# Optimization experiments

Measured on AMD Instinct MI355X. Metric: run time of the kernel, lower is better.

The kernel has to match this reference:

```python
import jax, jax.numpy as jnp
import numpy as np

GRID_SHAPE = (96, 96, 96)
GRID_LOWER = np.array([-1.2, -1.2, -1.2], dtype=np.float32)
GRID_STEPS = np.array([0.025, 0.025, 0.025], dtype=np.float32)
BIG = 1e10  # sentinel for cells outside an SDF's volume (min-combine ignores them)


def setup_inputs() -> dict:
    key = jax.random.key(0)
    k1, k2, k3, k4, k5 = jax.random.split(key, 5)
    M, S = 16, 64        # SDF library size, per-SDF resolution S^3
    B, N = 2, 8          # scenes, SDF instances per scene
    sdfs = jax.random.normal(k1, (M, S * S * S), dtype=jnp.float32)
    sdf_shapes = jnp.full((M, 3), S, dtype=jnp.int32)
    indices = jax.random.randint(k2, (B, N), 0, M, dtype=jnp.int32)
    trans = jax.random.uniform(k3, (B, N, 3), minval=-1.0, maxval=1.0)
    quat = jax.random.normal(k4, (B, N, 4))
    quat = quat / jnp.linalg.norm(quat, axis=-1, keepdims=True)
    sdf_poses = jnp.concatenate([trans, quat], axis=-1).astype(jnp.float32)
    sdf_widths = (0.02 * (1.0 + 0.2 * jax.random.uniform(k5, (B, N, 3)))).astype(jnp.float32)
    return {"sdfs": sdfs, "sdf_shapes": sdf_shapes, "indices": indices,
            "sdf_poses": sdf_poses, "sdf_widths": sdf_widths}


def _rotate_inv(q, v):
    # rotate v by the inverse (conjugate) of unit quaternion q = (x, y, z, w)
    u = -q[..., :3]
    w = q[..., 3:4]
    uv = jnp.cross(u, v)
    return v + 2.0 * jnp.cross(u, uv + w * v)


def reference(sdfs, sdf_shapes, indices, sdf_poses, sdf_widths):
    B, N = indices.shape
    GX, GY, GZ = GRID_SHAPE
    lower = jnp.asarray(GRID_LOWER)
    steps = jnp.asarray(GRID_STEPS)
    # world coordinates of grid cell centers: [GX, GY, GZ, 3]
    mesh = jnp.stack(jnp.meshgrid(jnp.arange(GX), jnp.arange(GY), jnp.arange(GZ),
                                  indexing='ij'), axis=-1).astype(jnp.float32)
    p = lower + (mesh + 0.5) * steps

    t = sdf_poses[..., :3]                                     # [B, N, 3]
    q = sdf_poses[..., 3:]
    q = q / jnp.linalg.norm(q, axis=-1, keepdims=True)         # [B, N, 4]

    # transform grid points into each SDF's local frame: [B, N, GX, GY, GZ, 3]
    d = p[None, None] - t[:, :, None, None, None, :]
    local = _rotate_inv(q[:, :, None, None, None, :], d)

    shp = sdf_shapes[indices]                                  # [B, N, 3] int
    shpf = shp.astype(local.dtype)[:, :, None, None, None, :]
    # continuous voxel coords, samples at cell centers
    g = local / sdf_widths[:, :, None, None, None, :] - 0.5
    inside = jnp.all((g >= 0.0) & (g <= shpf - 1.0), axis=-1)  # [B, N, GX, GY, GZ]
    f = jnp.clip(g, 0.0, shpf - 1.0)
    i0 = jnp.floor(f).astype(jnp.int32)
    frac = f - i0.astype(f.dtype)

    SX = shp[..., 0][:, :, None, None, None]
    SY = shp[..., 1][:, :, None, None, None]
    SZ = shp[..., 2][:, :, None, None, None]
    sdf_flat = sdfs[indices]                                   # [B, N, D]

    acc = jnp.zeros((B, N, GX, GY, GZ), dtype=sdfs.dtype)
    for dx in (0, 1):
        for dy in (0, 1):
            for dz in (0, 1):
                ii = jnp.minimum(i0[..., 0] + dx, SX - 1)
                jj = jnp.minimum(i0[..., 1] + dy, SY - 1)
                kk = jnp.minimum(i0[..., 2] + dz, SZ - 1)
                w = ((frac[..., 0] if dx else 1.0 - frac[..., 0]) *
                     (frac[..., 1] if dy else 1.0 - frac[..., 1]) *
                     (frac[..., 2] if dz else 1.0 - frac[..., 2]))
                flat = (ii * SY + jj) * SZ + kk
                vals = jnp.take_along_axis(sdf_flat, flat.reshape(B, N, -1),
                                           axis=2).reshape(B, N, GX, GY, GZ)
                acc = acc + w * vals

    per_sdf = jnp.where(inside, acc, BIG)
    return jnp.min(per_sdf, axis=1)                            # [B, GX, GY, GZ]
```

## Files before the change

kernel.cpp:

```cpp
#include <hip/hip_runtime.h>

#define GXD 96
#define GYD 96
#define GZD 96
#define PTS_PER_B (GXD * GYD * GZD)
#define BXC 8
#define BYC 8
#define BZC 8
#define GXB (GXD / BXC)
#define GYB (GYD / BYC)
#define GZB (GZD / BZC)
#define BLOCKS_PER_B (GXB * GYB * GZB)
#define RECSZ 56
#define BIGF 1e10f
#define GLOWER -1.2f
#define GSTEP 0.025f
#define EPS_G 1e-2f

__device__ __forceinline__ void rot_inv(float qx, float qy, float qz, float qw,
                                        float dx, float dy, float dz,
                                        float& rx, float& ry, float& rz)
{
    float ux = -qx, uy = -qy, uz = -qz;
    float uvx = uy * dz - uz * dy;
    float uvy = uz * dx - ux * dz;
    float uvz = ux * dy - uy * dx;
    float t2x = uvx + qw * dx;
    float t2y = uvy + qw * dy;
    float t2z = uvz + qw * dz;
    rx = dx + 2.0f * (uy * t2z - uz * t2y);
    ry = dy + 2.0f * (uz * t2x - ux * t2z);
    rz = dz + 2.0f * (ux * t2y - uy * t2x);
}

__device__ __forceinline__ float next_up(float a) { return __uint_as_float(__float_as_uint(a) + 1u); }
__device__ __forceinline__ float next_dn(float a) { return __uint_as_float(__float_as_uint(a) - 1u); }

__device__ float exact_lo(float w, float t)
{
    float a = t * w;
    while (a / w < t)            a = next_up(a);
    while (next_dn(a) / w >= t)  a = next_dn(a);
    return a;
}

__device__ float exact_hi(float w, float L)
{
    float a = L * w;
    while (a / w > L)            a = next_dn(a);
    while (next_up(a) / w <= L)  a = next_up(a);
    return a;
}

__global__ void prep_v9(const int* __restrict__ shapes,
                        const int* __restrict__ indices,
                        const float* __restrict__ poses,
                        const float* __restrict__ widths,
                        float* __restrict__ rec,
                        int BN, int sdf_stride)
{
    int bn = blockIdx.x * blockDim.x + threadIdx.x;
    if (bn >= BN) return;
    int m = indices[bn];
    const float* pp = poses + (size_t)bn * 7;
    float tx = pp[0], ty = pp[1], tz = pp[2];
    float qx = pp[3], qy = pp[4], qz = pp[5], qw = pp[6];
    float nrm = sqrtf(qx * qx + qy * qy + qz * qz + qw * qw);
    qx = qx / nrm; qy = qy / nrm; qz = qz / nrm; qw = qw / nrm;

    float wx = widths[bn * 3 + 0], wy = widths[bn * 3 + 1], wz = widths[bn * 3 + 2];
    int SX = shapes[m * 3 + 0], SY = shapes[m * 3 + 1], SZ = shapes[m * 3 + 2];
    float mx = (float)(SX - 1), my = (float)(SY - 1), mz = (float)(SZ - 1);

    float Ax = exact_lo(wx, 0.5f), Ay = exact_lo(wy, 0.5f), Az = exact_lo(wz, 0.5f);
    float Bx = exact_hi(wx, mx + 0.5f), By = exact_hi(wy, my + 0.5f), Bz = exact_hi(wz, mz + 0.5f);

    float xx = qx * qx, yy = qy * qy, zz = qz * qz;
    float xy = qx * qy, xz = qx * qz, yz = qy * qz;
    float wqx = qw * qx, wqy = qw * qy, wqz = qw * qz;
    float R00 = 1.0f - 2.0f * (yy + zz), R01 = 2.0f * (xy - wqz), R02 = 2.0f * (xz + wqy);
    float R10 = 2.0f * (xy + wqz), R11 = 1.0f - 2.0f * (xx + zz), R12 = 2.0f * (yz - wqx);
    float R20 = 2.0f * (xz - wqy), R21 = 2.0f * (yz + wqx), R22 = 1.0f - 2.0f * (xx + yy);

    float cx = 0.5f * (Ax + Bx), cy = 0.5f * (Ay + By), cz = 0.5f * (Az + Bz);
    float hx = 0.5f * (Bx - Ax), hy = 0.5f * (By - Ay), hz = 0.5f * (Bz - Az);
    const float MARG = 2e-3f;
    float wcx = tx + R00 * cx + R01 * cy + R02 * cz;
    float wcy = ty + R10 * cx + R11 * cy + R12 * cz;
    float wcz = tz + R20 * cx + R21 * cy + R22 * cz;
    float ex = fabsf(R00) * hx + fabsf(R01) * hy + fabsf(R02) * hz + MARG;
    float ey = fabsf(R10) * hx + fabsf(R11) * hy + fabsf(R12) * hz + MARG;
    float ez = fabsf(R20) * hx + fabsf(R21) * hy + fabsf(R22) * hz + MARG;

    float iwx = 1.0f / wx, iwy = 1.0f / wy, iwz = 1.0f / wz;
    float Mg0x = iwx * R00, Mg1x = iwx * R10, Mg2x = iwx * R20;
    float Mg0y = iwy * R01, Mg1y = iwy * R11, Mg2y = iwy * R21;
    float Mg0z = iwz * R02, Mg1z = iwz * R12, Mg2z = iwz * R22;
    float Cgx = -0.5f - (Mg0x * tx + Mg1x * ty + Mg2x * tz);
    float Cgy = -0.5f - (Mg0y * tx + Mg1y * ty + Mg2y * tz);
    float Cgz = -0.5f - (Mg0z * tx + Mg1z * ty + Mg2z * tz);

    float* r = rec + (size_t)bn * RECSZ;
    r[0] = tx;  r[1] = ty;  r[2] = tz;
    r[3] = qx;  r[4] = qy;  r[5] = qz;  r[6] = qw;
    r[7] = iwx; r[8] = iwy; r[9] = iwz;
    r[10] = mx; r[11] = my; r[12] = mz;
    r[13] = Ax; r[14] = Ay; r[15] = Az;
    r[16] = Bx; r[17] = By; r[18] = Bz;
    int* ri = (int*)r;
    ri[19] = m * sdf_stride;
    ri[20] = SX; ri[21] = SY; ri[22] = SZ;
    r[23] = 0.0f;
    r[24] = wcx - ex; r[25] = wcy - ey; r[26] = wcz - ez;
    r[27] = wcx + ex; r[28] = wcy + ey; r[29] = wcz + ez;
    r[30] = 0.0f; r[31] = 0.0f;
    r[32] = Mg0x; r[33] = Mg1x; r[34] = Mg2x;
    r[35] = Mg0y; r[36] = Mg1y; r[37] = Mg2y;
    r[38] = Mg0z; r[39] = Mg1z; r[40] = Mg2z;
    r[41] = Cgx; r[42] = Cgy; r[43] = Cgz;
    r[44] = mx + EPS_G; r[45] = my + EPS_G; r[46] = mz + EPS_G;
    r[47] = 0.0f;
    r[48] = mx - EPS_G; r[49] = my - EPS_G; r[50] = mz - EPS_G;
    r[51] = 0.0f; r[52] = 0.0f; r[53] = 0.0f; r[54] = 0.0f; r[55] = 0.0f;
}

struct __attribute__((aligned(4))) F2 { float lo, hi; };

__device__ __forceinline__ float trilerp_g(const float* __restrict__ sd,
                                           float gx, float gy, float gz,
                                           float mx, float my, float mz,
                                           int SX, int SY, int SZ)
{
    float fx = fminf(fmaxf(gx, 0.0f), mx);
    float fy = fminf(fmaxf(gy, 0.0f), my);
    float fz = fminf(fmaxf(gz, 0.0f), mz);
    int i0x = (int)fx, i0y = (int)fy, i0z = (int)fz;
    float frx = fx - (float)i0x;
    float fry = fy - (float)i0y;
    float frz = fz - (float)i0z;
    int i1x = min(i0x + 1, SX - 1);
    int i1y = min(i0y + 1, SY - 1);

    int zb = min(i0z, max(SZ - 2, 0));
    bool at0 = (i0z == zb);

    int b00 = (i0x * SY + i0y) * SZ + zb;
    int b01 = (i0x * SY + i1y) * SZ + zb;
    int b10 = (i1x * SY + i0y) * SZ + zb;
    int b11 = (i1x * SY + i1y) * SZ + zb;

    F2 p00 = *(const F2*)(sd + b00);
    F2 p01 = *(const F2*)(sd + b01);
    F2 p10 = *(const F2*)(sd + b10);
    F2 p11 = *(const F2*)(sd + b11);

    float v000 = at0 ? p00.lo : p00.hi, v001 = p00.hi;
    float v010 = at0 ? p01.lo : p01.hi, v011 = p01.hi;
    float v100 = at0 ? p10.lo : p10.hi, v101 = p10.hi;
    float v110 = at0 ? p11.lo : p11.hi, v111 = p11.hi;

    float c00 = v000 + frz * (v001 - v000);
    float c01 = v010 + frz * (v011 - v010);
    float c10 = v100 + frz * (v101 - v100);
    float c11 = v110 + frz * (v111 - v110);
    float c0 = c00 + fry * (c01 - c00);
    float c1 = c10 + fry * (c11 - c10);
    return c0 + frx * (c1 - c0);
}

__device__ __forceinline__ void eval_point(const float* __restrict__ r,
                                           const float* __restrict__ sdfs,
                                           float sgx, float sgy, float sgz,
                                           float px, float py, float pz,
                                           float& best)
{
    bool wide = (sgx >= -EPS_G) & (sgx <= r[44]) &
                (sgy >= -EPS_G) & (sgy <= r[45]) &
                (sgz >= -EPS_G) & (sgz <= r[46]);
    if (!wide) return;

    bool narrow = (sgx >= EPS_G) & (sgx <= r[48]) &
                  (sgy >= EPS_G) & (sgy <= r[49]) &
                  (sgz >= EPS_G) & (sgz <= r[50]);

    float gx = sgx, gy = sgy, gz = sgz;
    bool inside = true;
    if (!narrow) {
        float dx = px - r[0], dy = py - r[1], dz = pz - r[2];
        float rx, ry, rz;
        rot_inv(r[3], r[4], r[5], r[6], dx, dy, dz, rx, ry, rz);
        inside = (rx >= r[13]) & (rx <= r[16]) &
                 (ry >= r[14]) & (ry <= r[17]) &
                 (rz >= r[15]) & (rz <= r[18]);
        gx = rx * r[7] - 0.5f;
        gy = ry * r[8] - 0.5f;
        gz = rz * r[9] - 0.5f;
    }
    if (inside) {
        const int* ri = (const int*)r;
        float v = trilerp_g(sdfs + ri[19], gx, gy, gz,
                            r[10], r[11], r[12],
                            ri[20], ri[21], ri[22]);
        best = fminf(best, v);
    }
}

__global__ __launch_bounds__(256) void sdf_grid_v9(
    const float* __restrict__ sdfs,
    const float* __restrict__ rec,
    float* __restrict__ out,
    int N)
{
    int bidx = blockIdx.x;
    int b = blockIdx.y;
    int zb = bidx % GZB;
    int yb = (bidx / GZB) % GYB;
    int xb = bidx / (GZB * GYB);

    int t = threadIdx.x;
    int lane = t & 63;
    int lz = lane & 3;
    int ly = (lane >> 2) & 3;
    int lx = lane >> 4;
    int wx = (t >> 6) & 1;
    int wy = t >> 7;

    int cx = xb * BXC + wx * 4 + lx;
    int cy = yb * BYC + wy * 4 + ly;
    int cz = zb * BZC + lz * 2;

    float px  = GLOWER + ((float)cx + 0.5f) * GSTEP;
    float py  = GLOWER + ((float)cy + 0.5f) * GSTEP;
    float pz0 = GLOWER + ((float)cz + 0.5f) * GSTEP;
    float pz1 = GLOWER + ((float)(cz + 1) + 0.5f) * GSTEP;

    size_t out_idx = (size_t)b * PTS_PER_B + ((size_t)cx * GYD + cy) * GZD + cz;

    float bxl = GLOWER + ((float)(xb * BXC) + 0.5f) * GSTEP;
    float bxh = GLOWER + ((float)(xb * BXC + BXC - 1) + 0.5f) * GSTEP;
    float byl = GLOWER + ((float)(yb * BYC) + 0.5f) * GSTEP;
    float byh = GLOWER + ((float)(yb * BYC + BYC - 1) + 0.5f) * GSTEP;
    float bzl = GLOWER + ((float)(zb * BZC) + 0.5f) * GSTEP;
    float bzh = GLOWER + ((float)(zb * BZC + BZC - 1) + 0.5f) * GSTEP;

    bool lok = false;
    if (lane < N) {
        const float* r = rec + (size_t)(b * N + lane) * RECSZ;
        lok = (bxh >= r[24]) & (bxl <= r[27]) &
              (byh >= r[25]) & (byl <= r[28]) &
              (bzh >= r[26]) & (bzl <= r[29]);
    }
    unsigned int msk = (unsigned int)__ballot(lok);

    if (msk == 0u) {
        *(float2*)(out + out_idx) = make_float2(BIGF, BIGF);
        return;
    }

    float bestA = BIGF, bestB = BIGF;

    for (int n = 0; n < N; ++n) {
        if (!((msk >> n) & 1u)) continue;

        const float* r = rec + (size_t)(b * N + n) * RECSZ;

        float sgx = fmaf(r[32], px, fmaf(r[33], py, fmaf(r[34], pz0, r[41])));
        float sgy = fmaf(r[35], px, fmaf(r[36], py, fmaf(r[37], pz0, r[42])));
        float sgz = fmaf(r[38], px, fmaf(r[39], py, fmaf(r[40], pz0, r[43])));
        float dgx = GSTEP * r[34];
        float dgy = GSTEP * r[37];
        float dgz = GSTEP * r[40];

        eval_point(r, sdfs, sgx, sgy, sgz, px, py, pz0, bestA);
        eval_point(r, sdfs, sgx + dgx, sgy + dgy, sgz + dgz, px, py, pz1, bestB);
    }

    *(float2*)(out + out_idx) = make_float2(bestA, bestB);
}

__global__ __launch_bounds__(256) void sdf_grid_kernel(
    const float* __restrict__ sdfs,
    const int*   __restrict__ sdf_shapes,
    const int*   __restrict__ indices,
    const float* __restrict__ poses,
    const float* __restrict__ widths,
    float*       __restrict__ out,
    int total, int N, int sdf_stride)
{
    int idx = blockIdx.x * blockDim.x + threadIdx.x;
    if (idx >= total) return;
    int z = idx % GZD;
    int y = (idx / GZD) % GYD;
    int x = (idx / (GZD * GYD)) % GXD;
    int b = idx / (GZD * GYD * GXD);
    float px = GLOWER + ((float)x + 0.5f) * GSTEP;
    float py = GLOWER + ((float)y + 0.5f) * GSTEP;
    float pz = GLOWER + ((float)z + 0.5f) * GSTEP;
    float best = BIGF;
    for (int n = 0; n < N; ++n) {
        int bn = b * N + n;
        int m  = indices[bn];
        const float* pp = poses + (size_t)bn * 7;
        float tx = pp[0], ty = pp[1], tz = pp[2];
        float qx = pp[3], qy = pp[4], qz = pp[5], qw = pp[6];
        float nrm = sqrtf(qx * qx + qy * qy + qz * qz + qw * qw);
        qx = qx / nrm; qy = qy / nrm; qz = qz / nrm; qw = qw / nrm;
        float dx = px - tx, dy = py - ty, dz = pz - tz;
        float rx, ry, rz;
        rot_inv(qx, qy, qz, qw, dx, dy, dz, rx, ry, rz);
        const float* ww = widths + (size_t)bn * 3;
        float gx = rx / ww[0] - 0.5f;
        float gy = ry / ww[1] - 0.5f;
        float gz = rz / ww[2] - 0.5f;
        int SX = sdf_shapes[m * 3 + 0];
        int SY = sdf_shapes[m * 3 + 1];
        int SZ = sdf_shapes[m * 3 + 2];
        float mx = (float)(SX - 1), my = (float)(SY - 1), mz = (float)(SZ - 1);
        bool inside = (gx >= 0.0f) && (gx <= mx) &&
                      (gy >= 0.0f) && (gy <= my) &&
                      (gz >= 0.0f) && (gz <= mz);
        float fx = fminf(fmaxf(gx, 0.0f), mx);
        float fy = fminf(fmaxf(gy, 0.0f), my);
        float fz = fminf(fmaxf(gz, 0.0f), mz);
        int i0x = (int)floorf(fx), i0y = (int)floorf(fy), i0z = (int)floorf(fz);
        float frx = fx - (float)i0x, fry = fy - (float)i0y, frz = fz - (float)i0z;
        int i1x = min(i0x + 1, SX - 1);
        int i1y = min(i0y + 1, SY - 1);
        int i1z = min(i0z + 1, SZ - 1);
        const float* sd = sdfs + (size_t)m * sdf_stride;
        int b00 = (i0x * SY + i0y) * SZ;
        int b01 = (i0x * SY + i1y) * SZ;
        int b10 = (i1x * SY + i0y) * SZ;
        int b11 = (i1x * SY + i1y) * SZ;
        float v000 = sd[b00 + i0z], v001 = sd[b00 + i1z];
        float v010 = sd[b01 + i0z], v011 = sd[b01 + i1z];
        float v100 = sd[b10 + i0z], v101 = sd[b10 + i1z];
        float v110 = sd[b11 + i0z], v111 = sd[b11 + i1z];
        float wx0 = 1.0f - frx, wx1 = frx;
        float wy0 = 1.0f - fry, wy1 = fry;
        float wz0 = 1.0f - frz, wz1 = frz;
        float acc = wx0 * wy0 * wz0 * v000 + wx0 * wy0 * wz1 * v001
                  + wx0 * wy1 * wz0 * v010 + wx0 * wy1 * wz1 * v011
                  + wx1 * wy0 * wz0 * v100 + wx1 * wy0 * wz1 * v101
                  + wx1 * wy1 * wz0 * v110 + wx1 * wy1 * wz1 * v111;
        float val = inside ? acc : BIGF;
        best = fminf(best, val);
    }
    out[idx] = best;
}

extern "C" void kernel_launch(void* const* d_in, const int* in_sizes, int n_in,
                              void* d_out, int out_size, void* d_ws, size_t ws_size,
                              hipStream_t stream) {
    const float* sdfs    = (const float*)d_in[0];
    const int*   shapes  = (const int*)d_in[1];
    const int*   indices = (const int*)d_in[2];
    const float* poses   = (const float*)d_in[3];
    const float* widths  = (const float*)d_in[4];
    float*       out     = (float*)d_out;

    int M = in_sizes[1] / 3;
    int sdf_stride = in_sizes[0] / M;
    int B = out_size / PTS_PER_B;
    int N = in_sizes[2] / B;
    int BN = B * N;

    size_t ws_needed = (size_t)BN * RECSZ * sizeof(float);

    if (ws_size >= ws_needed && N <= 32 && (PTS_PER_B % 512) == 0) {
        float* rec = (float*)d_ws;
        prep_v9<<<(BN + 63) / 64, 64, 0, stream>>>(
            shapes, indices, poses, widths, rec, BN, sdf_stride);
        dim3 grid(BLOCKS_PER_B, B);
        sdf_grid_v9<<<grid, 256, 0, stream>>>(sdfs, rec, out, N);
    } else {
        int total = out_size;
        int blocks = (total + 255) / 256;
        sdf_grid_kernel<<<blocks, 256, 0, stream>>>(
            sdfs, shapes, indices, poses, widths, out, total, N, sdf_stride);
    }
}
```

Before: 24.85 us.

## Fuse per-instance prep into grid kernel via shared memory, four z-points per thread

Removes the separate prep kernel launch. Each block now recomputes the per-instance records into shared memory and reads them from LDS instead of global memory. The block shrinks to 128 threads, and each thread evaluates four consecutive z cells with incremental grid coordinates and writes one float4. The exact ulp-stepped bound computation is replaced by a division-based inside test, and every block redundantly recomputes the records, which adds a sync and per-block setup work.

```diff
diff --git a/kernel.cpp b/kernel.cpp
--- a/kernel.cpp
+++ b/kernel.cpp
@@ -11,11 +11,13 @@
 #define GYB (GYD / BYC)
 #define GZB (GZD / BZC)
 #define BLOCKS_PER_B (GXB * GYB * GZB)
-#define RECSZ 56
+#define MAXN 16
+#define RECL 44
 #define BIGF 1e10f
 #define GLOWER -1.2f
 #define GSTEP 0.025f
 #define EPS_G 1e-2f
+
 
 __device__ __forceinline__ void rot_inv(float qx, float qy, float qz, float qw,
                                         float dx, float dy, float dz,
@@ -33,97 +35,6 @@
     rz = dz + 2.0f * (ux * t2y - uy * t2x);
 }
 
-__device__ __forceinline__ float next_up(float a) { return __uint_as_float(__float_as_uint(a) + 1u); }
-__device__ __forceinline__ float next_dn(float a) { return __uint_as_float(__float_as_uint(a) - 1u); }
-
-__device__ float exact_lo(float w, float t)
-{
-    float a = t * w;
-    while (a / w < t)            a = next_up(a);
-    while (next_dn(a) / w >= t)  a = next_dn(a);
-    return a;
-}
-
-__device__ float exact_hi(float w, float L)
-{
-    float a = L * w;
-    while (a / w > L)            a = next_dn(a);
-    while (next_up(a) / w <= L)  a = next_up(a);
-    return a;
-}
-
-__global__ void prep_v9(const int* __restrict__ shapes,
-                        const int* __restrict__ indices,
-                        const float* __restrict__ poses,
-                        const float* __restrict__ widths,
-                        float* __restrict__ rec,
-                        int BN, int sdf_stride)
-{
-    int bn = blockIdx.x * blockDim.x + threadIdx.x;
-    if (bn >= BN) return;
-    int m = indices[bn];
-    const float* pp = poses + (size_t)bn * 7;
-    float tx = pp[0], ty = pp[1], tz = pp[2];
-    float qx = pp[3], qy = pp[4], qz = pp[5], qw = pp[6];
-    float nrm = sqrtf(qx * qx + qy * qy + qz * qz + qw * qw);
-    qx = qx / nrm; qy = qy / nrm; qz = qz / nrm; qw = qw / nrm;
-
-    float wx = widths[bn * 3 + 0], wy = widths[bn * 3 + 1], wz = widths[bn * 3 + 2];
-    int SX = shapes[m * 3 + 0], SY = shapes[m * 3 + 1], SZ = shapes[m * 3 + 2];
-    float mx = (float)(SX - 1), my = (float)(SY - 1), mz = (float)(SZ - 1);
-
-    float Ax = exact_lo(wx, 0.5f), Ay = exact_lo(wy, 0.5f), Az = exact_lo(wz, 0.5f);
-    float Bx = exact_hi(wx, mx + 0.5f), By = exact_hi(wy, my + 0.5f), Bz = exact_hi(wz, mz + 0.5f);
-
-    float xx = qx * qx, yy = qy * qy, zz = qz * qz;
-    float xy = qx * qy, xz = qx * qz, yz = qy * qz;
-    float wqx = qw * qx, wqy = qw * qy, wqz = qw * qz;
-    float R00 = 1.0f - 2.0f * (yy + zz), R01 = 2.0f * (xy - wqz), R02 = 2.0f * (xz + wqy);
-    float R10 = 2.0f * (xy + wqz), R11 = 1.0f - 2.0f * (xx + zz), R12 = 2.0f * (yz - wqx);
-    float R20 = 2.0f * (xz - wqy), R21 = 2.0f * (yz + wqx), R22 = 1.0f - 2.0f * (xx + yy);
-
-    float cx = 0.5f * (Ax + Bx), cy = 0.5f * (Ay + By), cz = 0.5f * (Az + Bz);
-    float hx = 0.5f * (Bx - Ax), hy = 0.5f * (By - Ay), hz = 0.5f * (Bz - Az);
-    const float MARG = 2e-3f;
-    float wcx = tx + R00 * cx + R01 * cy + R02 * cz;
-    float wcy = ty + R10 * cx + R11 * cy + R12 * cz;
-    float wcz = tz + R20 * cx + R21 * cy + R22 * cz;
-    float ex = fabsf(R00) * hx + fabsf(R01) * hy + fabsf(R02) * hz + MARG;
-    float ey = fabsf(R10) * hx + fabsf(R11) * hy + fabsf(R12) * hz + MARG;
-    float ez = fabsf(R20) * hx + fabsf(R21) * hy + fabsf(R22) * hz + MARG;
-
-    float iwx = 1.0f / wx, iwy = 1.0f / wy, iwz = 1.0f / wz;
-    float Mg0x = iwx * R00, Mg1x = iwx * R10, Mg2x = iwx * R20;
-    float Mg0y = iwy * R01, Mg1y = iwy * R11, Mg2y = iwy * R21;
-    float Mg0z = iwz * R02, Mg1z = iwz * R12, Mg2z = iwz * R22;
-    float Cgx = -0.5f - (Mg0x * tx + Mg1x * ty + Mg2x * tz);
-    float Cgy = -0.5f - (Mg0y * tx + Mg1y * ty + Mg2y * tz);
-    float Cgz = -0.5f - (Mg0z * tx + Mg1z * ty + Mg2z * tz);
-
-    float* r = rec + (size_t)bn * RECSZ;
-    r[0] = tx;  r[1] = ty;  r[2] = tz;
-    r[3] = qx;  r[4] = qy;  r[5] = qz;  r[6] = qw;
-    r[7] = iwx; r[8] = iwy; r[9] = iwz;
-    r[10] = mx; r[11] = my; r[12] = mz;
-    r[13] = Ax; r[14] = Ay; r[15] = Az;
-    r[16] = Bx; r[17] = By; r[18] = Bz;
-    int* ri = (int*)r;
-    ri[19] = m * sdf_stride;
-    ri[20] = SX; ri[21] = SY; ri[22] = SZ;
-    r[23] = 0.0f;
-    r[24] = wcx - ex; r[25] = wcy - ey; r[26] = wcz - ez;
-    r[27] = wcx + ex; r[28] = wcy + ey; r[29] = wcz + ez;
-    r[30] = 0.0f; r[31] = 0.0f;
-    r[32] = Mg0x; r[33] = Mg1x; r[34] = Mg2x;
-    r[35] = Mg0y; r[36] = Mg1y; r[37] = Mg2y;
-    r[38] = Mg0z; r[39] = Mg1z; r[40] = Mg2z;
-    r[41] = Cgx; r[42] = Cgy; r[43] = Cgz;
-    r[44] = mx + EPS_G; r[45] = my + EPS_G; r[46] = mz + EPS_G;
-    r[47] = 0.0f;
-    r[48] = mx - EPS_G; r[49] = my - EPS_G; r[50] = mz - EPS_G;
-    r[51] = 0.0f; r[52] = 0.0f; r[53] = 0.0f; r[54] = 0.0f; r[55] = 0.0f;
-}
-
 struct __attribute__((aligned(4))) F2 { float lo, hi; };
 
 __device__ __forceinline__ float trilerp_g(const float* __restrict__ sd,
@@ -174,14 +85,14 @@
                                            float px, float py, float pz,
                                            float& best)
 {
-    bool wide = (sgx >= -EPS_G) & (sgx <= r[44]) &
-                (sgy >= -EPS_G) & (sgy <= r[45]) &
-                (sgz >= -EPS_G) & (sgz <= r[46]);
+    bool wide = (sgx >= -EPS_G) & (sgx <= r[25]) &
+                (sgy >= -EPS_G) & (sgy <= r[26]) &
+                (sgz >= -EPS_G) & (sgz <= r[27]);
     if (!wide) return;
 
-    bool narrow = (sgx >= EPS_G) & (sgx <= r[48]) &
-                  (sgy >= EPS_G) & (sgy <= r[49]) &
-                  (sgz >= EPS_G) & (sgz <= r[50]);
+    bool narrow = (sgx >= EPS_G) & (sgx <= r[28]) &
+                  (sgy >= EPS_G) & (sgy <= r[29]) &
+                  (sgz >= EPS_G) & (sgz <= r[30]);
 
     float gx = sgx, gy = sgy, gz = sgz;
     bool inside = true;
@@ -189,93 +100,163 @@
         float dx = px - r[0], dy = py - r[1], dz = pz - r[2];
         float rx, ry, rz;
         rot_inv(r[3], r[4], r[5], r[6], dx, dy, dz, rx, ry, rz);
-        inside = (rx >= r[13]) & (rx <= r[16]) &
-                 (ry >= r[14]) & (ry <= r[17]) &
-                 (rz >= r[15]) & (rz <= r[18]);
-        gx = rx * r[7] - 0.5f;
-        gy = ry * r[8] - 0.5f;
-        gz = rz * r[9] - 0.5f;
+        gx = rx / r[7] - 0.5f;
+        gy = ry / r[8] - 0.5f;
+        gz = rz / r[9] - 0.5f;
+        inside = (gx >= 0.0f) & (gx <= r[10]) &
+                 (gy >= 0.0f) & (gy <= r[11]) &
+                 (gz >= 0.0f) & (gz <= r[12]);
     }
     if (inside) {
         const int* ri = (const int*)r;
-        float v = trilerp_g(sdfs + ri[19], gx, gy, gz,
+        float v = trilerp_g(sdfs + ri[37], gx, gy, gz,
                             r[10], r[11], r[12],
-                            ri[20], ri[21], ri[22]);
+                            ri[38], ri[39], ri[40]);
         best = fminf(best, v);
     }
 }
 
-__global__ __launch_bounds__(256) void sdf_grid_v9(
+__global__ __launch_bounds__(128) void sdf_grid_v11(
     const float* __restrict__ sdfs,
-    const float* __restrict__ rec,
-    float* __restrict__ out,
-    int N)
-{
+    const int*   __restrict__ shapes,
+    const int*   __restrict__ indices,
+    const float* __restrict__ poses,
+    const float* __restrict__ widths,
+    float*       __restrict__ out,
+    int N, int sdf_stride)
+{
+    __shared__ float srec[MAXN][RECL];
+
     int bidx = blockIdx.x;
     int b = blockIdx.y;
-    int zb = bidx % GZB;
-    int yb = (bidx / GZB) % GYB;
-    int xb = bidx / (GZB * GYB);
+    int zbk = bidx % GZB;
+    int ybk = (bidx / GZB) % GYB;
+    int xbk = bidx / (GZB * GYB);
 
     int t = threadIdx.x;
+
+    if (t < N) {
+        int bn = b * N + t;
+        int m = indices[bn];
+        const float* pp = poses + (size_t)bn * 7;
+        float tx = pp[0], ty = pp[1], tz = pp[2];
+        float qx = pp[3], qy = pp[4], qz = pp[5], qw = pp[6];
+        float nrm = sqrtf(qx * qx + qy * qy + qz * qz + qw * qw);
+        qx = qx / nrm; qy = qy / nrm; qz = qz / nrm; qw = qw / nrm;
+
+        float wx = widths[bn * 3 + 0], wy = widths[bn * 3 + 1], wz = widths[bn * 3 + 2];
+        int SX = shapes[m * 3 + 0], SY = shapes[m * 3 + 1], SZ = shapes[m * 3 + 2];
+        float mx = (float)(SX - 1), my = (float)(SY - 1), mz = (float)(SZ - 1);
+
+        float xx = qx * qx, yy = qy * qy, zz = qz * qz;
+        float xy = qx * qy, xz = qx * qz, yz = qy * qz;
+        float wqx = qw * qx, wqy = qw * qy, wqz = qw * qz;
+        float R00 = 1.0f - 2.0f * (yy + zz), R01 = 2.0f * (xy - wqz), R02 = 2.0f * (xz + wqy);
+        float R10 = 2.0f * (xy + wqz), R11 = 1.0f - 2.0f * (xx + zz), R12 = 2.0f * (yz - wqx);
+        float R20 = 2.0f * (xz - wqy), R21 = 2.0f * (yz + wqx), R22 = 1.0f - 2.0f * (xx + yy);
+
+        float Axa = 0.5f * wx, Aya = 0.5f * wy, Aza = 0.5f * wz;
+        float Bxa = (mx + 0.5f) * wx, Bya = (my + 0.5f) * wy, Bza = (mz + 0.5f) * wz;
+        float cx = 0.5f * (Axa + Bxa), cy = 0.5f * (Aya + Bya), cz = 0.5f * (Aza + Bza);
+        float hx = 0.5f * (Bxa - Axa), hy = 0.5f * (Bya - Aya), hz = 0.5f * (Bza - Aza);
+        const float MARG = 2e-3f;
+        float wcx = tx + R00 * cx + R01 * cy + R02 * cz;
+        float wcy = ty + R10 * cx + R11 * cy + R12 * cz;
+        float wcz = tz + R20 * cx + R21 * cy + R22 * cz;
+        float ex = fabsf(R00) * hx + fabsf(R01) * hy + fabsf(R02) * hz + MARG;
+        float ey = fabsf(R10) * hx + fabsf(R11) * hy + fabsf(R12) * hz + MARG;
+        float ez = fabsf(R20) * hx + fabsf(R21) * hy + fabsf(R22) * hz + MARG;
+
+        float iwx = 1.0f / wx, iwy = 1.0f / wy, iwz = 1.0f / wz;
+        float Mg0x = iwx * R00, Mg1x = iwx * R10, Mg2x = iwx * R20;
+        float Mg0y = iwy * R01, Mg1y = iwy * R11, Mg2y = iwy * R21;
+        float Mg0z = iwz * R02, Mg1z = iwz * R12, Mg2z = iwz * R22;
+        float Cgx = -0.5f - (Mg0x * tx + Mg1x * ty + Mg2x * tz);
+        float Cgy = -0.5f - (Mg0y * tx + Mg1y * ty + Mg2y * tz);
+        float Cgz = -0.5f - (Mg0z * tx + Mg1z * ty + Mg2z * tz);
+
+        float* r = srec[t];
+        r[0] = tx;  r[1] = ty;  r[2] = tz;
+        r[3] = qx;  r[4] = qy;  r[5] = qz;  r[6] = qw;
+        r[7] = wx;  r[8] = wy;  r[9] = wz;
+        r[10] = mx; r[11] = my; r[12] = mz;
+        r[13] = Mg0x; r[14] = Mg1x; r[15] = Mg2x;
+        r[16] = Mg0y; r[17] = Mg1y; r[18] = Mg2y;
+        r[19] = Mg0z; r[20] = Mg1z; r[21] = Mg2z;
+        r[22] = Cgx; r[23] = Cgy; r[24] = Cgz;
+        r[25] = mx + EPS_G; r[26] = my + EPS_G; r[27] = mz + EPS_G;
+        r[28] = mx - EPS_G; r[29] = my - EPS_G; r[30] = mz - EPS_G;
+        r[31] = wcx - ex; r[32] = wcy - ey; r[33] = wcz - ez;
+        r[34] = wcx + ex; r[35] = wcy + ey; r[36] = wcz + ez;
+        int* ri = (int*)r;
+        ri[37] = m * sdf_stride;
+        ri[38] = SX; ri[39] = SY; ri[40] = SZ;
+    }
+    __syncthreads();
+
     int lane = t & 63;
-    int lz = lane & 3;
-    int ly = (lane >> 2) & 3;
-    int lx = lane >> 4;
-    int wx = (t >> 6) & 1;
-    int wy = t >> 7;
-
-    int cx = xb * BXC + wx * 4 + lx;
-    int cy = yb * BYC + wy * 4 + ly;
-    int cz = zb * BZC + lz * 2;
+    int lyy = lane & 7;
+    int lxx = lane >> 3;
+    int wz4 = (t >> 6) & 1;
+
+    int cx = xbk * BXC + lxx;
+    int cy = ybk * BYC + lyy;
+    int cz0 = zbk * BZC + wz4 * 4;
 
     float px  = GLOWER + ((float)cx + 0.5f) * GSTEP;
     float py  = GLOWER + ((float)cy + 0.5f) * GSTEP;
-    float pz0 = GLOWER + ((float)cz + 0.5f) * GSTEP;
-    float pz1 = GLOWER + ((float)(cz + 1) + 0.5f) * GSTEP;
-
-    size_t out_idx = (size_t)b * PTS_PER_B + ((size_t)cx * GYD + cy) * GZD + cz;
-
-    float bxl = GLOWER + ((float)(xb * BXC) + 0.5f) * GSTEP;
-    float bxh = GLOWER + ((float)(xb * BXC + BXC - 1) + 0.5f) * GSTEP;
-    float byl = GLOWER + ((float)(yb * BYC) + 0.5f) * GSTEP;
-    float byh = GLOWER + ((float)(yb * BYC + BYC - 1) + 0.5f) * GSTEP;
-    float bzl = GLOWER + ((float)(zb * BZC) + 0.5f) * GSTEP;
-    float bzh = GLOWER + ((float)(zb * BZC + BZC - 1) + 0.5f) * GSTEP;
+    float pz0 = GLOWER + ((float)cz0 + 0.5f) * GSTEP;
+    float pz1 = GLOWER + ((float)(cz0 + 1) + 0.5f) * GSTEP;
+    float pz2 = GLOWER + ((float)(cz0 + 2) + 0.5f) * GSTEP;
+    float pz3 = GLOWER + ((float)(cz0 + 3) + 0.5f) * GSTEP;
+
+    size_t out_idx = (size_t)b * PTS_PER_B + ((size_t)cx * GYD + cy) * GZD + cz0;
+
+    float bxl = GLOWER + ((float)(xbk * BXC) + 0.5f) * GSTEP;
+    float bxh = GLOWER + ((float)(xbk * BXC + 7) + 0.5f) * GSTEP;
+    float byl = GLOWER + ((float)(ybk * BYC) + 0.5f) * GSTEP;
+    float byh = GLOWER + ((float)(ybk * BYC + 7) + 0.5f) * GSTEP;
+    float bzl = GLOWER + ((float)(zbk * BZC + wz4 * 4) + 0.5f) * GSTEP;
+    float bzh = GLOWER + ((float)(zbk * BZC + wz4 * 4 + 3) + 0.5f) * GSTEP;
 
     bool lok = false;
     if (lane < N) {
-        const float* r = rec + (size_t)(b * N + lane) * RECSZ;
-        lok = (bxh >= r[24]) & (bxl <= r[27]) &
-              (byh >= r[25]) & (byl <= r[28]) &
-              (bzh >= r[26]) & (bzl <= r[29]);
+        const float* r = srec[lane];
+        lok = (bxh >= r[31]) & (bxl <= r[34]) &
+              (byh >= r[32]) & (byl <= r[35]) &
+              (bzh >= r[33]) & (bzl <= r[36]);
     }
     unsigned int msk = (unsigned int)__ballot(lok);
 
     if (msk == 0u) {
-        *(float2*)(out + out_idx) = make_float2(BIGF, BIGF);
+        *(float4*)(out + out_idx) = make_float4(BIGF, BIGF, BIGF, BIGF);
         return;
     }
 
-    float bestA = BIGF, bestB = BIGF;
+    float b0 = BIGF, b1 = BIGF, b2 = BIGF, b3 = BIGF;
 
     for (int n = 0; n < N; ++n) {
         if (!((msk >> n) & 1u)) continue;
 
-        const float* r = rec + (size_t)(b * N + n) * RECSZ;
-
-        float sgx = fmaf(r[32], px, fmaf(r[33], py, fmaf(r[34], pz0, r[41])));
-        float sgy = fmaf(r[35], px, fmaf(r[36], py, fmaf(r[37], pz0, r[42])));
-        float sgz = fmaf(r[38], px, fmaf(r[39], py, fmaf(r[40], pz0, r[43])));
-        float dgx = GSTEP * r[34];
-        float dgy = GSTEP * r[37];
-        float dgz = GSTEP * r[40];
-
-        eval_point(r, sdfs, sgx, sgy, sgz, px, py, pz0, bestA);
-        eval_point(r, sdfs, sgx + dgx, sgy + dgy, sgz + dgz, px, py, pz1, bestB);
-    }
-
-    *(float2*)(out + out_idx) = make_float2(bestA, bestB);
+        const float* r = srec[n];
+
+        float sgx = fmaf(r[13], px, fmaf(r[14], py, fmaf(r[15], pz0, r[22])));
+        float sgy = fmaf(r[16], px, fmaf(r[17], py, fmaf(r[18], pz0, r[23])));
+        float sgz = fmaf(r[19], px, fmaf(r[20], py, fmaf(r[21], pz0, r[24])));
+        float dgx = GSTEP * r[15];
+        float dgy = GSTEP * r[18];
+        float dgz = GSTEP * r[21];
+
+        eval_point(r, sdfs, sgx, sgy, sgz, px, py, pz0, b0);
+        float s1x = sgx + dgx, s1y = sgy + dgy, s1z = sgz + dgz;
+        eval_point(r, sdfs, s1x, s1y, s1z, px, py, pz1, b1);
+        float s2x = s1x + dgx, s2y = s1y + dgy, s2z = s1z + dgz;
+        eval_point(r, sdfs, s2x, s2y, s2z, px, py, pz2, b2);
+        float s3x = s2x + dgx, s3y = s2y + dgy, s3z = s2z + dgz;
+        eval_point(r, sdfs, s3x, s3y, s3z, px, py, pz3, b3);
+    }
+
+    *(float4*)(out + out_idx) = make_float4(b0, b1, b2, b3);
 }
 
 __global__ __launch_bounds__(256) void sdf_grid_kernel(
@@ -363,16 +344,11 @@
     int sdf_stride = in_sizes[0] / M;
     int B = out_size / PTS_PER_B;
     int N = in_sizes[2] / B;
-    int BN = B * N;
-
-    size_t ws_needed = (size_t)BN * RECSZ * sizeof(float);
-
-    if (ws_size >= ws_needed && N <= 32 && (PTS_PER_B % 512) == 0) {
-        float* rec = (float*)d_ws;
-        prep_v9<<<(BN + 63) / 64, 64, 0, stream>>>(
-            shapes, indices, poses, widths, rec, BN, sdf_stride);
+
+    if (N <= MAXN && (PTS_PER_B % 512) == 0) {
         dim3 grid(BLOCKS_PER_B, B);
-        sdf_grid_v9<<<grid, 256, 0, stream>>>(sdfs, rec, out, N);
+        sdf_grid_v11<<<grid, 128, 0, stream>>>(
+            sdfs, shapes, indices, poses, widths, out, N, sdf_stride);
     } else {
         int total = out_size;
         int blocks = (total + 255) / 256;
```

Result: faster. 23.84 us (-4.0%).
